# Kernel tuning notes

Hardware: AMD Instinct MI355X
Metric: run time of the kernel (lower is better)

The kernel has to match this reference:

```python
import jax, jax.numpy as jnp
import numpy as np

N = 20000   # nodes per type per hop
E = 200000  # edges per relation per hop
H = 512     # node_feature_hid_len
FU = 512    # raw user feature len
FI = 256    # raw item feature len
NUM_RES = 2
NUM_DNN = 2


def setup_inputs() -> dict:
    key = jax.random.key(0)
    ks = iter(jax.random.split(key, 64))
    p = lambda shape: jax.random.normal(next(ks), shape, dtype=jnp.float32) * 0.05
    inp = {}
    # features per hop per type
    for h in range(3):
        inp[f'feat_user_h{h}'] = jax.random.normal(next(ks), (N, FU), dtype=jnp.float32)
        inp[f'feat_item_h{h}'] = jax.random.normal(next(ks), (N, FI), dtype=jnp.float32)
    del inp['feat_user_h2_']; 


def _unused():
    pass

# rebuild setup_inputs cleanly (above stub replaced)

def setup_inputs() -> dict:
    key = jax.random.key(0)
    ks = iter(jax.random.split(key, 64))
    p = lambda shape: jax.random.normal(next(ks), shape, dtype=jnp.float32) * 0.05
    inp = {}
    for h in range(3):
        inp[f'feat_user_h{h}'] = jax.random.normal(next(ks), (N, FU), dtype=jnp.float32)
        inp[f'feat_item_h{h}'] = jax.random.normal(next(ks), (N, FI), dtype=jnp.float32)
    for name in ('edges_UI_h0', 'edges_IU_h0', 'edges_UI_h1', 'edges_IU_h1'):
        inp[name] = jax.random.randint(next(ks), (2, E), 0, N, dtype=jnp.int32)
    # per-node-type input transforms
    inp['W_user'] = p((FU, H)); inp['b_user'] = jnp.zeros((H,), jnp.float32)
    inp['W_item'] = p((FI, H)); inp['b_item'] = jnp.zeros((H,), jnp.float32)
    # per-relation GATConv params, stacked over 2 relations [UI, IU]
    inp['gat_feat_W'] = p((2, H, H)); inp['gat_feat_b'] = jnp.zeros((2, H), jnp.float32)
    inp['gat_att_w'] = p((2, 2 * H)); inp['gat_att_b'] = jnp.zeros((2,), jnp.float32)
    inp['gat_bias'] = jnp.zeros((2, H), jnp.float32)
    # Res_DNN params
    inp['prep_W'] = p((H, H)); inp['prep_b'] = jnp.zeros((H,), jnp.float32)
    inp['dnn_W'] = p((NUM_RES, NUM_DNN, H, H)); inp['dnn_b'] = jnp.zeros((NUM_RES, NUM_DNN, H), jnp.float32)
    inp['dnn_ln_g'] = jnp.ones((NUM_RES, NUM_DNN, H), jnp.float32); inp['dnn_ln_b'] = jnp.zeros((NUM_RES, NUM_DNN, H), jnp.float32)
    inp['res_ln_g'] = jnp.ones((NUM_RES, H), jnp.float32); inp['res_ln_b'] = jnp.zeros((NUM_RES, H), jnp.float32)
    inp['cls_W'] = p((H, 1)); inp['cls_b'] = jnp.zeros((1,), jnp.float32)
    return inp


def _ln(x, g, b, eps=1e-5):
    mu = jnp.mean(x, axis=-1, keepdims=True)
    var = jnp.mean((x - mu) ** 2, axis=-1, keepdims=True)
    return (x - mu) * jax.lax.rsqrt(var + eps) * g + b


def _gat(head_h, tail_h, edges, fW, fb, aw, ab, bias):
    # GATConv: feat_linear on both sides, tanh edge attention, per-source-row
    # sparse softmax, scatter-weighted sum of transformed tail features.
    s = head_h @ fW + fb            # [Nh, H]
    t = tail_h @ fW + fb            # [Nt, H]
    src, tgt = edges[0], edges[1]
    # att(cat([s_e, t_e])) split into per-node scores (same math as concat @ aw)
    e = jnp.tanh((s @ aw[:H])[src] + (t @ aw[H:])[tgt] + ab)  # [E]
    nh = head_h.shape[0]
    m = jax.ops.segment_max(e, src, num_segments=nh)
    ex = jnp.exp(e - m[src])
    den = jax.ops.segment_sum(ex, src, num_segments=nh)
    alpha = ex / den[src]
    hp = jax.ops.segment_sum(alpha[:, None] * t[tgt], src, num_segments=nh)
    return hp + bias


def _forward(feat_user_h0, feat_item_h0, feat_user_h1, feat_item_h1,
             feat_user_h2, feat_item_h2,
             W_user, b_user, W_item, b_item,
             gat_feat_W, gat_feat_b, gat_att_w, gat_att_b, gat_bias,
             prep_W, prep_b, dnn_W, dnn_b, dnn_ln_g, dnn_ln_b,
             res_ln_g, res_ln_b, cls_W, cls_b,
             edges_UI_h0, edges_IU_h0, edges_UI_h1, edges_IU_h1):
    def gat(r, head, tail, edges):
        return _gat(head, tail, edges, gat_feat_W[r], gat_feat_b[r],
                    gat_att_w[r], gat_att_b[r], gat_bias[r])
    # hop 2 (deepest): transformed source features
    su = feat_user_h2 @ W_user + b_user
    si = feat_item_h2 @ W_item + b_item
    # hop 1
    hu = feat_user_h1 @ W_user + b_user
    hi = feat_item_h1 @ W_item + b_item
    su_new = (hu + gat(0, hu, si, edges_UI_h1)) * 0.5  # mean of [self, UI agg]
    si_new = (hi + gat(1, hi, su, edges_IU_h1)) * 0.5
    su, si = su_new, si_new
    # hop 0
    hu = feat_user_h0 @ W_user + b_user
    hi = feat_item_h0 @ W_item + b_item
    su_new = (hu + gat(0, hu, si, edges_UI_h0)) * 0.5
    su = su_new  # target node type = 'user' (first key)
    # Res_DNN head
    x = su @ prep_W + prep_b
    for r in range(NUM_RES):
        sc = x
        for d in range(NUM_DNN):
            x = _ln(jnp.tanh(x @ dnn_W[r, d] + dnn_b[r, d]), dnn_ln_g[r, d], dnn_ln_b[r, d])
        x = _ln(jnp.tanh(sc + x), res_ln_g[r], res_ln_b[r])
    return jax.nn.sigmoid(x @ cls_W + cls_b)  # [N, 1]


def reference(feat_user_h0, feat_item_h0, feat_user_h1, feat_item_h1,
              feat_user_h2, feat_item_h2,
              edges_UI_h0, edges_IU_h0, edges_UI_h1, edges_IU_h1,
              W_user, b_user, W_item, b_item,
              gat_feat_W, gat_feat_b, gat_att_w, gat_att_b, gat_bias,
              prep_W, prep_b, dnn_W, dnn_b, dnn_ln_g, dnn_ln_b,
              res_ln_g, res_ln_b, cls_W, cls_b):
    return _forward(feat_user_h0, feat_item_h0, feat_user_h1, feat_item_h1,
                    feat_user_h2, feat_item_h2,
                    W_user, b_user, W_item, b_item,
                    gat_feat_W, gat_feat_b, gat_att_w, gat_att_b, gat_bias,
                    prep_W, prep_b, dnn_W, dnn_b, dnn_ln_g, dnn_ln_b,
                    res_ln_g, res_ln_b, cls_W, cls_b,
                    edges_UI_h0, edges_IU_h0, edges_UI_h1, edges_IU_h1)
```

## Files before the change

kernel.cpp:

```cpp
#include <hip/hip_runtime.h>
#include <math.h>

#define NN 20000
#define NE 200000
#define HH 512

typedef __attribute__((ext_vector_type(8))) short short8v;
typedef __attribute__((ext_vector_type(4))) float f32x4;

__device__ inline short f2bf(float f) {
    union { float f; unsigned u; } v; v.f = f;
    unsigned r = (v.u + 0x7fffu + ((v.u >> 16) & 1u)) >> 16;
    return (short)r;
}
__device__ inline float bf2f(short s) {
    union { unsigned u; float f; } v;
    v.u = ((unsigned)(unsigned short)s) << 16;
    return v.f;
}

__device__ inline void gload_lds16(const void* g, void* l) {
    __builtin_amdgcn_global_load_lds(
        (const __attribute__((address_space(1))) void*)g,
        (__attribute__((address_space(3))) void*)l, 16, 0, 0);
}

__global__ __launch_bounds__(256)
void f2b_kernel(const float* __restrict__ src, short* __restrict__ dst, int n8)
{
    int i = blockIdx.x * 256 + threadIdx.x;
    if (i >= n8) return;
    const float4* p = (const float4*)src + (size_t)i * 2;
    float4 a = p[0], b = p[1];
    short8v s;
    s[0] = f2bf(a.x); s[1] = f2bf(a.y); s[2] = f2bf(a.z); s[3] = f2bf(a.w);
    s[4] = f2bf(b.x); s[5] = f2bf(b.y); s[6] = f2bf(b.z); s[7] = f2bf(b.w);
    ((short8v*)dst)[i] = s;
}

__global__ __launch_bounds__(256)
void wtr_kernel(const float* __restrict__ src, short* __restrict__ dst,
                int K, int Ncols)
{
    __shared__ float t[32][33];
    int bx = blockIdx.x * 32;
    int by = blockIdx.y * 32;
    int tx = threadIdx.x, ty = threadIdx.y;
    for (int i = ty; i < 32; i += 8)
        t[i][tx] = src[(size_t)(by + i) * Ncols + bx + tx];
    __syncthreads();
    for (int i = ty; i < 32; i += 8)
        dst[(size_t)(bx + i) * K + by + tx] = f2bf(t[tx][i]);
}

__global__ __launch_bounds__(256)
void mfma_lin(const short* __restrict__ X, const short* __restrict__ WT,
              const float* __restrict__ bias, float* __restrict__ outF,
              short* __restrict__ outB, int M, int K)
{
    __shared__ short8v pool[4096];

    const int tid = threadIdx.x;
    const int lane = tid & 63;
    const int w = tid >> 6;

    const int nby = (M + 127) >> 7;
    const int nwg = nby << 2;
    const int q = nwg >> 3, r = nwg & 7;
    int id = blockIdx.x;
    int xcd = id & 7, wi = id >> 3;
    int wgid = (xcd < r ? xcd * (q + 1) : r * (q + 1) + (xcd - r) * q) + wi;
    const int col0 = (wgid & 3) * 128;
    const int row0 = (wgid >> 2) * 128;

    const int wr = (w >> 1) * 64;
    const int wc = (w & 1) * 64;

    const short* gsrc[8];
#pragma unroll
    for (int g = 0; g < 8; ++g) {
        int p = w * 512 + g * 64 + lane;
        if (p < 1024) {
            int row = p >> 3;
            int c = (p & 7) ^ (row & 7);
            int ga = row0 + row; if (ga >= M) ga = M - 1;
            gsrc[g] = X + (size_t)ga * K + c * 8;
        } else {
            int qq = p - 1024;
            int col = qq >> 3;
            int c = (qq & 7) ^ (col & 7);
            gsrc[g] = WT + (size_t)(col0 + col) * K + c * 8;
        }
    }

    int ar[2][4], br[2][4];
#pragma unroll
    for (int kk = 0; kk < 2; ++kk) {
#pragma unroll
        for (int i = 0; i < 4; ++i) {
            int rr = wr + i * 16 + (lane & 15);
            ar[kk][i] = rr * 8 + ((kk * 4 + (lane >> 4)) ^ (rr & 7));
            int nn = wc + i * 16 + (lane & 15);
            br[kk][i] = 1024 + nn * 8 + ((kk * 4 + (lane >> 4)) ^ (nn & 7));
        }
    }

    f32x4 acc[4][4];
#pragma unroll
    for (int i = 0; i < 4; ++i)
#pragma unroll
        for (int j = 0; j < 4; ++j)
            acc[i][j] = (f32x4){0.f, 0.f, 0.f, 0.f};

    auto stage = [&](int buf, int kk) {
        short8v* base = pool + buf * 2048 + w * 512;
#pragma unroll
        for (int g = 0; g < 8; ++g)
            gload_lds16(gsrc[g] + kk, base + g * 64);
    };

    const int nt = K >> 6;
    stage(0, 0);
    if (nt > 1) stage(1, 64);
    int cur = 0;
    for (int t = 0; t < nt; ++t) {
        if (t + 1 < nt) asm volatile("s_waitcnt vmcnt(8)" ::: "memory");
        else            asm volatile("s_waitcnt vmcnt(0)" ::: "memory");
        __builtin_amdgcn_s_barrier();
        const short8v* S = pool + cur * 2048;
#pragma unroll
        for (int kk = 0; kk < 2; ++kk) {
            short8v af[4], bf[4];
#pragma unroll
            for (int i = 0; i < 4; ++i) af[i] = S[ar[kk][i]];
#pragma unroll
            for (int j = 0; j < 4; ++j) bf[j] = S[br[kk][j]];
#pragma unroll
            for (int i = 0; i < 4; ++i)
#pragma unroll
                for (int j = 0; j < 4; ++j)
                    acc[i][j] = __builtin_amdgcn_mfma_f32_16x16x32_bf16(af[i], bf[j], acc[i][j], 0, 0, 0);
        }
        __builtin_amdgcn_s_barrier();
        if (t + 2 < nt) stage(cur, (t + 2) * 64);
        cur ^= 1;
    }

    float bj[4];
#pragma unroll
    for (int j = 0; j < 4; ++j)
        bj[j] = bias[col0 + wc + j * 16 + (lane & 15)];

    if (outF) {
#pragma unroll
        for (int i = 0; i < 4; ++i) {
#pragma unroll
            for (int rr = 0; rr < 4; ++rr) {
                int row = row0 + wr + i * 16 + (lane >> 4) * 4 + rr;
                if (row < M) {
                    float* op = outF + (size_t)row * HH + col0 + wc + (lane & 15);
#pragma unroll
                    for (int j = 0; j < 4; ++j) op[j * 16] = acc[i][j][rr] + bj[j];
                }
            }
        }
    }
    if (outB) {
        short* lds = (short*)pool + w * 4608;
#pragma unroll
        for (int i = 0; i < 4; ++i)
#pragma unroll
            for (int rr = 0; rr < 4; ++rr) {
                int lrow = i * 16 + (lane >> 4) * 4 + rr;
#pragma unroll
                for (int j = 0; j < 4; ++j)
                    lds[lrow * 72 + j * 16 + (lane & 15)] = f2bf(acc[i][j][rr] + bj[j]);
            }
#pragma unroll
        for (int k = 0; k < 8; ++k) {
            int lr = (lane >> 3) + 8 * k;
            int lc = (lane & 7) * 8;
            int grow = row0 + wr + lr;
            if (grow < M) {
                short8v vv = *(short8v*)(lds + lr * 72 + lc);
                *(short8v*)(outB + (size_t)grow * HH + col0 + wc + lc) = vv;
            }
        }
    }
}

__global__ __launch_bounds__(256)
void gat_pre_kernel(const float* __restrict__ fW, const float* __restrict__ fb,
                    const float* __restrict__ aw, float* __restrict__ uv,
                    float* __restrict__ s0t0)
{
    int row = blockIdx.x * 4 + (threadIdx.x >> 6);
    int lane = threadIdx.x & 63;
    const float4* ah = (const float4*)aw;
    const float4* at = (const float4*)(aw + HH);
    const float4* fp;
    if (row < 512)      fp = (const float4*)(fW + (size_t)row * HH);
    else if (row == 512) fp = (const float4*)fb;
    else return;
    float du = 0.f, dv = 0.f;
#pragma unroll
    for (int l = 0; l < 2; ++l) {
        int idx = lane * 2 + l;
        float4 f = fp[idx], a = ah[idx], b = at[idx];
        du += f.x*a.x + f.y*a.y + f.z*a.z + f.w*a.w;
        dv += f.x*b.x + f.y*b.y + f.z*b.z + f.w*b.w;
    }
#pragma unroll
    for (int m = 32; m >= 1; m >>= 1) {
        du += __shfl_xor(du, m);
        dv += __shfl_xor(dv, m);
    }
    if (lane == 0) {
        if (row < 512) { uv[row] = du; uv[512 + row] = dv; }
        else           { s0t0[0] = du; s0t0[1] = dv; }
    }
}

__global__ __launch_bounds__(256)
void rowdot2_kernel(const short* __restrict__ Hd, const short* __restrict__ Tl,
                    const float* __restrict__ uv, const float* __restrict__ s0t0,
                    float* __restrict__ ss, float* __restrict__ ts, int N)
{
    int row = blockIdx.x * 4 + (threadIdx.x >> 6);
    int lane = threadIdx.x & 63;
    if (row >= N) return;
    short8v h = ((const short8v*)(Hd + (size_t)row * HH))[lane];
    short8v t = ((const short8v*)(Tl + (size_t)row * HH))[lane];
    const float4* up = (const float4*)uv + lane * 2;
    const float4* vp = (const float4*)(uv + HH) + lane * 2;
    float4 u0 = up[0], u1 = up[1], v0 = vp[0], v1 = vp[1];
    float a = bf2f(h[0])*u0.x + bf2f(h[1])*u0.y + bf2f(h[2])*u0.z + bf2f(h[3])*u0.w
            + bf2f(h[4])*u1.x + bf2f(h[5])*u1.y + bf2f(h[6])*u1.z + bf2f(h[7])*u1.w;
    float b = bf2f(t[0])*v0.x + bf2f(t[1])*v0.y + bf2f(t[2])*v0.z + bf2f(t[3])*v0.w
            + bf2f(t[4])*v1.x + bf2f(t[5])*v1.y + bf2f(t[6])*v1.z + bf2f(t[7])*v1.w;
#pragma unroll
    for (int m = 32; m >= 1; m >>= 1) {
        a += __shfl_xor(a, m);
        b += __shfl_xor(b, m);
    }
    if (lane == 0) { ss[row] = a + s0t0[0]; ts[row] = b + s0t0[1]; }
}

__global__ __launch_bounds__(256)
void count2_kernel(const int* __restrict__ s0, const int* __restrict__ s1,
                   int* __restrict__ c0, int* __restrict__ c1, int E)
{
    int i = blockIdx.x * blockDim.x + threadIdx.x;
    if (i < E) atomicAdd(&c0[s0[i]], 1);
    else if (i < 2 * E) atomicAdd(&c1[s1[i - E]], 1);
}

__global__ __launch_bounds__(1024)
void scan2_kernel(const int* __restrict__ c0, const int* __restrict__ c1,
                  int* __restrict__ o0, int* __restrict__ o1,
                  int* __restrict__ u0, int* __restrict__ u1, int n)
{
    const int* counts = blockIdx.x ? c1 : c0;
    int* offs = blockIdx.x ? o1 : o0;
    int* curs = blockIdx.x ? u1 : u0;
    __shared__ int part[1024];
    const int tid = threadIdx.x;
    const int CH = (n + 1023) / 1024;
    const int base = tid * CH;
    int s = 0;
    for (int i = 0; i < CH; ++i) {
        int idx = base + i;
        if (idx < n) s += counts[idx];
    }
    part[tid] = s;
    __syncthreads();
    for (int d = 1; d < 1024; d <<= 1) {
        int v = 0;
        if (tid >= d) v = part[tid - d];
        __syncthreads();
        if (tid >= d) part[tid] += v;
        __syncthreads();
    }
    int run = (tid == 0) ? 0 : part[tid - 1];
    for (int i = 0; i < CH; ++i) {
        int idx = base + i;
        if (idx < n) { offs[idx] = run; curs[idx] = run; run += counts[idx]; }
    }
    if (tid == 1023) offs[n] = run;
}

__global__ __launch_bounds__(256)
void fill_kernel(const int* __restrict__ src, const int* __restrict__ tgt,
                 const float* __restrict__ ss, const float* __restrict__ ts,
                 const float* __restrict__ ab_ptr, int* __restrict__ cursor,
                 int* __restrict__ tvals, float* __restrict__ wv, int E)
{
    int i = blockIdx.x * blockDim.x + threadIdx.x;
    if (i >= E) return;
    int s = src[i], t = tgt[i];
    int pos = atomicAdd(&cursor[s], 1);
    tvals[pos] = t;
    wv[pos] = expf(tanhf(ss[s] + ts[t] + ab_ptr[0]));
}

__global__ __launch_bounds__(256)
void gat_agg_kernel(const int* __restrict__ offs, const int* __restrict__ tvals,
                    const float* __restrict__ wv, const short* __restrict__ T,
                    const short* __restrict__ head, const float* __restrict__ gbias,
                    short* __restrict__ out, int N)
{
    int s = blockIdx.x * 4 + (threadIdx.x >> 6);
    int lane = threadIdx.x & 63;
    if (s >= N) return;
    const int beg = offs[s], end = offs[s + 1];
    float a[8];
#pragma unroll
    for (int q = 0; q < 8; ++q) a[q] = 0.f;
    float den = 0.f;

    int j = beg;
    for (; j + 4 <= end; j += 4) {
        int t0 = tvals[j], t1 = tvals[j + 1], t2 = tvals[j + 2], t3 = tvals[j + 3];
        float w0 = wv[j], w1 = wv[j + 1], w2 = wv[j + 2], w3 = wv[j + 3];
        short8v v0 = ((const short8v*)(T + (size_t)t0 * HH))[lane];
        short8v v1 = ((const short8v*)(T + (size_t)t1 * HH))[lane];
        short8v v2 = ((const short8v*)(T + (size_t)t2 * HH))[lane];
        short8v v3 = ((const short8v*)(T + (size_t)t3 * HH))[lane];
        den += w0 + w1 + w2 + w3;
#pragma unroll
        for (int q = 0; q < 8; ++q) {
            float acc = a[q];
            acc = fmaf(w0, bf2f(v0[q]), acc);
            acc = fmaf(w1, bf2f(v1[q]), acc);
            acc = fmaf(w2, bf2f(v2[q]), acc);
            acc = fmaf(w3, bf2f(v3[q]), acc);
            a[q] = acc;
        }
    }
    for (; j < end; ++j) {
        int t = tvals[j];
        float w = wv[j];
        short8v tv = ((const short8v*)(T + (size_t)t * HH))[lane];
        den += w;
#pragma unroll
        for (int q = 0; q < 8; ++q) a[q] = fmaf(w, bf2f(tv[q]), a[q]);
    }
    float inv = (den > 0.f) ? 1.f / den : 0.f;

    short8v h = ((const short8v*)(head + (size_t)s * HH))[lane];
    const float4* bp = (const float4*)gbias + lane * 2;
    float4 b0 = bp[0], b1 = bp[1];
    float bb[8] = {b0.x, b0.y, b0.z, b0.w, b1.x, b1.y, b1.z, b1.w};
    short8v o;
#pragma unroll
    for (int q = 0; q < 8; ++q)
        o[q] = f2bf((bf2f(h[q]) + a[q] * inv + bb[q]) * 0.5f);
    ((short8v*)(out + (size_t)s * HH))[lane] = o;
}

__global__ __launch_bounds__(256)
void tanh_ln_kernel(const short* __restrict__ Z, const float* __restrict__ res,
                    const float* __restrict__ g, const float* __restrict__ bta,
                    short* __restrict__ outB, float* __restrict__ outF,
                    const float* __restrict__ cWp, const float* __restrict__ cbp,
                    float* __restrict__ outCls, int N)
{
    int row = blockIdx.x * 4 + (threadIdx.x >> 6);
    int lane = threadIdx.x & 63;
    if (row >= N) return;
    short8v zv = ((const short8v*)(Z + (size_t)row * HH))[lane];
    float v[8];
    float sum = 0.f, sum2 = 0.f;
    float rr[8];
    if (res) {
        const float4* rp = (const float4*)(res + (size_t)row * HH) + lane * 2;
        float4 r0 = rp[0], r1 = rp[1];
        rr[0]=r0.x; rr[1]=r0.y; rr[2]=r0.z; rr[3]=r0.w;
        rr[4]=r1.x; rr[5]=r1.y; rr[6]=r1.z; rr[7]=r1.w;
    } else {
#pragma unroll
        for (int q = 0; q < 8; ++q) rr[q] = 0.f;
    }
#pragma unroll
    for (int q = 0; q < 8; ++q) {
        float t = tanhf(bf2f(zv[q]) + rr[q]);
        v[q] = t;
        sum += t;
        sum2 = fmaf(t, t, sum2);
    }
#pragma unroll
    for (int m = 32; m >= 1; m >>= 1) {
        sum  += __shfl_xor(sum, m);
        sum2 += __shfl_xor(sum2, m);
    }
    float mu  = sum * (1.f/HH);
    float var = sum2 * (1.f/HH) - mu*mu;
    float rs  = rsqrtf(var + 1e-5f);
    const float4* gp = (const float4*)g + lane * 2;
    const float4* bp = (const float4*)bta + lane * 2;
    float4 g0 = gp[0], g1 = gp[1], c0 = bp[0], c1 = bp[1];
    float gg[8] = {g0.x, g0.y, g0.z, g0.w, g1.x, g1.y, g1.z, g1.w};
    float cc[8] = {c0.x, c0.y, c0.z, c0.w, c1.x, c1.y, c1.z, c1.w};
    float o[8];
#pragma unroll
    for (int q = 0; q < 8; ++q) o[q] = (v[q]-mu)*rs*gg[q] + cc[q];
    if (outB) {
        short8v ob;
#pragma unroll
        for (int q = 0; q < 8; ++q) ob[q] = f2bf(o[q]);
        ((short8v*)(outB + (size_t)row * HH))[lane] = ob;
    }
    if (outF) {
        float4* op = (float4*)(outF + (size_t)row * HH) + lane * 2;
        op[0] = make_float4(o[0], o[1], o[2], o[3]);
        op[1] = make_float4(o[4], o[5], o[6], o[7]);
    }
    if (cWp) {
        const float4* wp = (const float4*)cWp + lane * 2;
        float4 w0 = wp[0], w1 = wp[1];
        float acc = o[0]*w0.x + o[1]*w0.y + o[2]*w0.z + o[3]*w0.w
                  + o[4]*w1.x + o[5]*w1.y + o[6]*w1.z + o[7]*w1.w;
#pragma unroll
        for (int m = 32; m >= 1; m >>= 1) acc += __shfl_xor(acc, m);
        if (lane == 0) outCls[row] = 1.f / (1.f + expf(-(acc + cbp[0])));
    }
}

extern "C" void kernel_launch(void* const* d_in, const int* in_sizes, int n_in,
                              void* d_out, int out_size, void* d_ws, size_t ws_size,
                              hipStream_t stream)
{
    (void)in_sizes; (void)n_in; (void)out_size; (void)ws_size;
    const int N = NN, E = NE, H = HH;
    const size_t NHf = (size_t)N * H;

    const float* fu0 = (const float*)d_in[0];
    const float* fi1 = (const float*)d_in[3];
    const float* fu2 = (const float*)d_in[4];
    const int* eUI0 = (const int*)d_in[6];
    const int* eIU1 = (const int*)d_in[9];
    const float* Wu  = (const float*)d_in[10];
    const float* bu  = (const float*)d_in[11];
    const float* Wi  = (const float*)d_in[12];
    const float* bi  = (const float*)d_in[13];
    const float* gfW = (const float*)d_in[14];
    const float* gfb = (const float*)d_in[15];
    const float* gaw = (const float*)d_in[16];
    const float* gab = (const float*)d_in[17];
    const float* gbias = (const float*)d_in[18];
    const float* prW = (const float*)d_in[19];
    const float* prb = (const float*)d_in[20];
    const float* dW  = (const float*)d_in[21];
    const float* db  = (const float*)d_in[22];
    const float* dlg = (const float*)d_in[23];
    const float* dlb = (const float*)d_in[24];
    const float* rlg = (const float*)d_in[25];
    const float* rlb = (const float*)d_in[26];
    const float* cW  = (const float*)d_in[27];
    const float* cb  = (const float*)d_in[28];

    float* B5   = (float*)d_ws;
    float* ssb  = B5 + NHf;
    float* tsb  = ssb + N;
    float* uv   = tsb + N;
    float* s0t0 = uv + 1024;
    float* wvb  = s0t0 + 4;
    int* counts0 = (int*)(wvb + E);
    int* counts1 = counts0 + N;
    int* offs0   = counts1 + N;
    int* offs1   = offs0 + N + 1;
    int* cur0    = offs1 + N + 1;
    int* cur1    = cur0 + N;
    int* tvals   = cur1 + N;
    size_t boff = (size_t)((char*)(tvals + E) - (char*)d_ws);
    boff = (boff + 15) & ~(size_t)15;
    short* S0    = (short*)((char*)d_ws + boff);
    short* SUHU  = S0 + 2 * NHf;
    short* XI1   = SUHU + 2 * NHf;
    short* HI    = XI1 + NHf / 2;
    short* SINEW = HI + NHf;
    short* T4    = SINEW + NHf;
    short* SUF   = T4 + NHf;
    short* WTu   = SUF + NHf;
    short* WTi   = WTu + 512 * 512;
    short* WTg0  = WTi + 512 * 256;
    short* WTg1  = WTg0 + 512 * 512;
    short* WTpr  = WTg1 + 512 * 512;
    short* WTd   = WTpr + 512 * 512;
    short* SU  = SUHU;
    short* HU0 = SUHU + NHf;
    short* XB  = SINEW;
    short* ZB  = SU;

    auto WTR = [&](const float* src, short* dst, int K) {
        hipLaunchKernelGGL(wtr_kernel, dim3(16, K / 32), dim3(32, 8), 0, stream,
                           src, dst, K, 512);
    };
    WTR(Wu, WTu, 512);
    WTR(Wi, WTi, 256);
    WTR(gfW, WTg0, 512);
    WTR(gfW + (size_t)H * H, WTg1, 512);
    WTR(prW, WTpr, 512);
    for (int k = 0; k < 4; ++k)
        WTR(dW + (size_t)k * H * H, WTd + (size_t)k * 512 * 512, 512);

    auto F2B = [&](const float* src, short* dst, size_t n) {
        int n8 = (int)(n / 8);
        hipLaunchKernelGGL(f2b_kernel, dim3((n8 + 255) / 256), dim3(256), 0, stream,
                           src, dst, n8);
    };

    hipMemsetAsync(counts0, 0, 2 * N * sizeof(int), stream);
    hipLaunchKernelGGL(count2_kernel, dim3((2 * E + 255) / 256), dim3(256), 0, stream,
                       eUI0, eIU1, counts0, counts1, E);
    hipLaunchKernelGGL(scan2_kernel, dim3(2), dim3(1024), 0, stream,
                       counts0, counts1, offs0, offs1, cur0, cur1, N);

    auto MLIN = [&](const short* X, const short* WT, const float* b,
                    float* oF, short* oB, int M, int K) {
        int nwg = ((M + 127) / 128) * 4;
        hipLaunchKernelGGL(mfma_lin, dim3(nwg), dim3(256), 0, stream,
                           X, WT, b, oF, oB, M, K);
    };
    const int rgrid = (N + 3) / 4;
    const int egrid = (E + 255) / 256;

    auto GAT = [&](int r, const short* headB, const short* tailB, const short* WTg,
                   const int* edges, int* offs, int* curs, short* outB) {
        hipLaunchKernelGGL(gat_pre_kernel, dim3(130), dim3(256), 0, stream,
                           gfW + (size_t)r * H * H, gfb + r * H, gaw + (size_t)r * 2 * H,
                           uv, s0t0);
        MLIN(tailB, WTg, gfb + r * H, nullptr, T4, N, 512);
        hipLaunchKernelGGL(rowdot2_kernel, dim3(rgrid), dim3(256), 0, stream,
                           headB, tailB, uv, s0t0, ssb, tsb, N);
        hipLaunchKernelGGL(fill_kernel, dim3(egrid), dim3(256), 0, stream,
                           edges, edges + E, ssb, tsb, gab + r, curs, tvals, wvb, E);
        hipLaunchKernelGGL(gat_agg_kernel, dim3(rgrid), dim3(256), 0, stream,
                           offs, tvals, wvb, T4, headB, gbias + (size_t)r * H, outB, N);
    };

    F2B(fu2, S0, NHf);
    F2B(fu0, S0 + NHf, NHf);
    F2B(fi1, XI1, NHf / 2);
    MLIN(S0, WTu, bu, nullptr, SUHU, 2 * N, 512);
    MLIN(XI1, WTi, bi, nullptr, HI, N, 256);
    GAT(1, HI, SU, WTg1, eIU1, offs1, cur1, SINEW);
    GAT(0, HU0, SINEW, WTg0, eUI0, offs0, cur0, SUF);

    MLIN(SUF, WTpr, prb, B5, XB, N, 512);
    for (int r = 0; r < 2; ++r) {
        for (int d = 0; d < 2; ++d) {
            MLIN(XB, WTd + (size_t)(r * 2 + d) * 512 * 512, db + (r * 2 + d) * H,
                 nullptr, ZB, N, 512);
            hipLaunchKernelGGL(tanh_ln_kernel, dim3(rgrid), dim3(256), 0, stream,
                               ZB, (const float*)nullptr, dlg + (r * 2 + d) * H,
                               dlb + (r * 2 + d) * H, XB, (float*)nullptr,
                               (const float*)nullptr, (const float*)nullptr,
                               (float*)nullptr, N);
        }
        if (r == 0) {
            hipLaunchKernelGGL(tanh_ln_kernel, dim3(rgrid), dim3(256), 0, stream,
                               XB, B5, rlg, rlb, XB, B5,
                               (const float*)nullptr, (const float*)nullptr,
                               (float*)nullptr, N);
        } else {
            hipLaunchKernelGGL(tanh_ln_kernel, dim3(rgrid), dim3(256), 0, stream,
                               XB, B5, rlg + H, rlb + H, (short*)nullptr,
                               (float*)nullptr, cW, cb, (float*)d_out, N);
        }
    }
}
```

Measured before the change: 561.3 us.

## Batch prep kernels, fuse rowdot into GEMM grid, fuse LN pairs, sort edge buckets

Merges the nine weight-transpose launches and three fp32-to-bf16 conversions into single launches, and runs both GAT attention-vector precomputes in one launch. The row-dot attention scores are computed by extra blocks appended to the GAT GEMM grid, so one launch is saved per relation. The second DNN tanh+LN is fused with the residual tanh+LN. The bf16 GEMM epilogue now stages a full 128x128 tile in LDS with a barrier so stores cover whole tiles. A new per-node sort of CSR buckets by edge index adds work to make the aggregation order deterministic, at the cost of an extra launch and memory traffic.

```diff
diff --git a/kernel.cpp b/kernel.cpp
--- a/kernel.cpp
+++ b/kernel.cpp
@@ -26,28 +26,48 @@
 }
 
 __global__ __launch_bounds__(256)
-void f2b_kernel(const float* __restrict__ src, short* __restrict__ dst, int n8)
+void f2b_all(const float* __restrict__ fu2, const float* __restrict__ fu0,
+             const float* __restrict__ fi1, short* __restrict__ S0,
+             short* __restrict__ XI1, int nh8)
 {
     int i = blockIdx.x * 256 + threadIdx.x;
-    if (i >= n8) return;
-    const float4* p = (const float4*)src + (size_t)i * 2;
+    const float* src; short* dst; int off;
+    if (i < nh8)            { src = fu2; dst = S0;                    off = i; }
+    else if (i < 2 * nh8)   { src = fu0; dst = S0 + (size_t)nh8 * 8;  off = i - nh8; }
+    else if (i < 2 * nh8 + nh8 / 2) { src = fi1; dst = XI1;           off = i - 2 * nh8; }
+    else return;
+    const float4* p = (const float4*)src + (size_t)off * 2;
     float4 a = p[0], b = p[1];
     short8v s;
     s[0] = f2bf(a.x); s[1] = f2bf(a.y); s[2] = f2bf(a.z); s[3] = f2bf(a.w);
     s[4] = f2bf(b.x); s[5] = f2bf(b.y); s[6] = f2bf(b.z); s[7] = f2bf(b.w);
-    ((short8v*)dst)[i] = s;
-}
-
-__global__ __launch_bounds__(256)
-void wtr_kernel(const float* __restrict__ src, short* __restrict__ dst,
-                int K, int Ncols)
+    ((short8v*)dst)[off] = s;
+}
+
+__global__ __launch_bounds__(256)
+void wtr_all(const float* __restrict__ Wu, const float* __restrict__ Wi,
+             const float* __restrict__ gfW, const float* __restrict__ prW,
+             const float* __restrict__ dW,
+             short* __restrict__ WTu, short* __restrict__ WTi,
+             short* __restrict__ WTg0, short* __restrict__ WTg1,
+             short* __restrict__ WTpr, short* __restrict__ WTd)
 {
     __shared__ float t[32][33];
+    int z = blockIdx.z;
+    const float* src; short* dst; int K;
+    if (z == 0)      { src = Wu;  dst = WTu;  K = 512; }
+    else if (z == 1) { src = Wi;  dst = WTi;  K = 256; }
+    else if (z == 2) { src = gfW; dst = WTg0; K = 512; }
+    else if (z == 3) { src = gfW + (size_t)512 * 512; dst = WTg1; K = 512; }
+    else if (z == 4) { src = prW; dst = WTpr; K = 512; }
+    else { src = dW + (size_t)(z - 5) * 512 * 512;
+           dst = WTd + (size_t)(z - 5) * 512 * 512; K = 512; }
+    int by = blockIdx.y * 32;
+    if (by >= K) return;
     int bx = blockIdx.x * 32;
-    int by = blockIdx.y * 32;
     int tx = threadIdx.x, ty = threadIdx.y;
     for (int i = ty; i < 32; i += 8)
-        t[i][tx] = src[(size_t)(by + i) * Ncols + bx + tx];
+        t[i][tx] = src[(size_t)(by + i) * 512 + bx + tx];
     __syncthreads();
     for (int i = ty; i < 32; i += 8)
         dst[(size_t)(bx + i) * K + by + tx] = f2bf(t[tx][i]);
@@ -56,7 +76,10 @@
 __global__ __launch_bounds__(256)
 void mfma_lin(const short* __restrict__ X, const short* __restrict__ WT,
               const float* __restrict__ bias, float* __restrict__ outF,
-              short* __restrict__ outB, int M, int K)
+              short* __restrict__ outB, int M, int K,
+              const short* __restrict__ rdH, const short* __restrict__ rdT,
+              const float* __restrict__ rduv, const float* __restrict__ rds0,
+              float* __restrict__ rdss, float* __restrict__ rdts, int rdN)
 {
     __shared__ short8v pool[4096];
 
@@ -66,8 +89,30 @@
 
     const int nby = (M + 127) >> 7;
     const int nwg = nby << 2;
+    int id = blockIdx.x;
+
+    if (id >= nwg) {
+        int row = (id - nwg) * 4 + w;
+        if (row >= rdN) return;
+        short8v h = ((const short8v*)(rdH + (size_t)row * HH))[lane];
+        short8v t = ((const short8v*)(rdT + (size_t)row * HH))[lane];
+        const float4* up = (const float4*)rduv + lane * 2;
+        const float4* vp = (const float4*)(rduv + HH) + lane * 2;
+        float4 u0 = up[0], u1 = up[1], v0 = vp[0], v1 = vp[1];
+        float a = bf2f(h[0])*u0.x + bf2f(h[1])*u0.y + bf2f(h[2])*u0.z + bf2f(h[3])*u0.w
+                + bf2f(h[4])*u1.x + bf2f(h[5])*u1.y + bf2f(h[6])*u1.z + bf2f(h[7])*u1.w;
+        float b = bf2f(t[0])*v0.x + bf2f(t[1])*v0.y + bf2f(t[2])*v0.z + bf2f(t[3])*v0.w
+                + bf2f(t[4])*v1.x + bf2f(t[5])*v1.y + bf2f(t[6])*v1.z + bf2f(t[7])*v1.w;
+#pragma unroll
+        for (int m = 32; m >= 1; m >>= 1) {
+            a += __shfl_xor(a, m);
+            b += __shfl_xor(b, m);
+        }
+        if (lane == 0) { rdss[row] = a + rds0[0]; rdts[row] = b + rds0[1]; }
+        return;
+    }
+
     const int q = nwg >> 3, r = nwg & 7;
-    int id = blockIdx.x;
     int xcd = id & 7, wi = id >> 3;
     int wgid = (xcd < r ? xcd * (q + 1) : r * (q + 1) + (xcd - r) * q) + wi;
     const int col0 = (wgid & 3) * 128;
@@ -166,40 +211,47 @@
         }
     }
     if (outB) {
-        short* lds = (short*)pool + w * 4608;
+        short* lt = (short*)pool;
 #pragma unroll
         for (int i = 0; i < 4; ++i)
 #pragma unroll
             for (int rr = 0; rr < 4; ++rr) {
-                int lrow = i * 16 + (lane >> 4) * 4 + rr;
+                int lrow = wr + i * 16 + (lane >> 4) * 4 + rr;
 #pragma unroll
                 for (int j = 0; j < 4; ++j)
-                    lds[lrow * 72 + j * 16 + (lane & 15)] = f2bf(acc[i][j][rr] + bj[j]);
+                    lt[lrow * 128 + wc + j * 16 + (lane & 15)] = f2bf(acc[i][j][rr] + bj[j]);
             }
+        __syncthreads();
 #pragma unroll
         for (int k = 0; k < 8; ++k) {
-            int lr = (lane >> 3) + 8 * k;
-            int lc = (lane & 7) * 8;
-            int grow = row0 + wr + lr;
+            int row = (tid >> 4) + 16 * k;
+            int seg = tid & 15;
+            int grow = row0 + row;
             if (grow < M) {
-                short8v vv = *(short8v*)(lds + lr * 72 + lc);
-                *(short8v*)(outB + (size_t)grow * HH + col0 + wc + lc) = vv;
+                short8v vv = *(short8v*)(lt + row * 128 + seg * 8);
+                *(short8v*)(outB + (size_t)grow * HH + col0 + seg * 8) = vv;
             }
         }
     }
 }
 
 __global__ __launch_bounds__(256)
-void gat_pre_kernel(const float* __restrict__ fW, const float* __restrict__ fb,
-                    const float* __restrict__ aw, float* __restrict__ uv,
-                    float* __restrict__ s0t0)
-{
+void gat_pre2(const float* __restrict__ gfW, const float* __restrict__ gfb,
+              const float* __restrict__ gaw, float* __restrict__ uvall,
+              float* __restrict__ s0t0all)
+{
+    int rrel = blockIdx.y;
+    const float* fW = gfW + (size_t)rrel * HH * HH;
+    const float* fb = gfb + rrel * HH;
+    const float* aw = gaw + (size_t)rrel * 2 * HH;
+    float* uv = uvall + rrel * 1024;
+    float* s0t0 = s0t0all + rrel * 4;
     int row = blockIdx.x * 4 + (threadIdx.x >> 6);
     int lane = threadIdx.x & 63;
     const float4* ah = (const float4*)aw;
     const float4* at = (const float4*)(aw + HH);
     const float4* fp;
-    if (row < 512)      fp = (const float4*)(fW + (size_t)row * HH);
+    if (row < 512)       fp = (const float4*)(fW + (size_t)row * HH);
     else if (row == 512) fp = (const float4*)fb;
     else return;
     float du = 0.f, dv = 0.f;
@@ -219,31 +271,6 @@
         if (row < 512) { uv[row] = du; uv[512 + row] = dv; }
         else           { s0t0[0] = du; s0t0[1] = dv; }
     }
-}
-
-__global__ __launch_bounds__(256)
-void rowdot2_kernel(const short* __restrict__ Hd, const short* __restrict__ Tl,
-                    const float* __restrict__ uv, const float* __restrict__ s0t0,
-                    float* __restrict__ ss, float* __restrict__ ts, int N)
-{
-    int row = blockIdx.x * 4 + (threadIdx.x >> 6);
-    int lane = threadIdx.x & 63;
-    if (row >= N) return;
-    short8v h = ((const short8v*)(Hd + (size_t)row * HH))[lane];
-    short8v t = ((const short8v*)(Tl + (size_t)row * HH))[lane];
-    const float4* up = (const float4*)uv + lane * 2;
-    const float4* vp = (const float4*)(uv + HH) + lane * 2;
-    float4 u0 = up[0], u1 = up[1], v0 = vp[0], v1 = vp[1];
-    float a = bf2f(h[0])*u0.x + bf2f(h[1])*u0.y + bf2f(h[2])*u0.z + bf2f(h[3])*u0.w
-            + bf2f(h[4])*u1.x + bf2f(h[5])*u1.y + bf2f(h[6])*u1.z + bf2f(h[7])*u1.w;
-    float b = bf2f(t[0])*v0.x + bf2f(t[1])*v0.y + bf2f(t[2])*v0.z + bf2f(t[3])*v0.w
-            + bf2f(t[4])*v1.x + bf2f(t[5])*v1.y + bf2f(t[6])*v1.z + bf2f(t[7])*v1.w;
-#pragma unroll
-    for (int m = 32; m >= 1; m >>= 1) {
-        a += __shfl_xor(a, m);
-        b += __shfl_xor(b, m);
-    }
-    if (lane == 0) { ss[row] = a + s0t0[0]; ts[row] = b + s0t0[1]; }
 }
 
 __global__ __launch_bounds__(256)
@@ -293,7 +320,8 @@
 void fill_kernel(const int* __restrict__ src, const int* __restrict__ tgt,
                  const float* __restrict__ ss, const float* __restrict__ ts,
                  const float* __restrict__ ab_ptr, int* __restrict__ cursor,
-                 int* __restrict__ tvals, float* __restrict__ wv, int E)
+                 int* __restrict__ tvals, float* __restrict__ wv,
+                 int* __restrict__ eidx, int E)
 {
     int i = blockIdx.x * blockDim.x + threadIdx.x;
     if (i >= E) return;
@@ -301,6 +329,40 @@
     int pos = atomicAdd(&cursor[s], 1);
     tvals[pos] = t;
     wv[pos] = expf(tanhf(ss[s] + ts[t] + ab_ptr[0]));
+    eidx[pos] = i;
+}
+
+__global__ __launch_bounds__(256)
+void sortbkt_kernel(const int* __restrict__ offs, int* __restrict__ tvals,
+                    float* __restrict__ wv, const int* __restrict__ eidx, int N)
+{
+    __shared__ int   lt[4][512];
+    __shared__ float lw[4][512];
+    int w = threadIdx.x >> 6, lane = threadIdx.x & 63;
+    int s = blockIdx.x * 4 + w;
+    if (s >= N) return;
+    int beg = offs[s], end = offs[s + 1];
+    int L = end - beg;
+    if (L <= 1) return;
+    if (L <= 64) {
+        int e = 0x7fffffff, t = 0; float fw = 0.f;
+        if (lane < L) { e = eidx[beg + lane]; t = tvals[beg + lane]; fw = wv[beg + lane]; }
+        int r = 0;
+        for (int k = 0; k < L; ++k) {
+            int ek = __shfl(e, k);
+            r += (ek < e) ? 1 : 0;
+        }
+        if (lane < L) { tvals[beg + r] = t; wv[beg + r] = fw; }
+    } else if (L <= 512) {
+        for (int j = lane; j < L; j += 64) { lt[w][j] = tvals[beg + j]; lw[w][j] = wv[beg + j]; }
+        asm volatile("s_waitcnt lgkmcnt(0) vmcnt(0)" ::: "memory");
+        for (int j = lane; j < L; j += 64) {
+            int e = eidx[beg + j];
+            int r = 0;
+            for (int k = 0; k < L; ++k) r += (eidx[beg + k] < e) ? 1 : 0;
+            tvals[beg + r] = lt[w][j]; wv[beg + r] = lw[w][j];
+        }
+    }
 }
 
 __global__ __launch_bounds__(256)
@@ -359,11 +421,9 @@
 }
 
 __global__ __launch_bounds__(256)
-void tanh_ln_kernel(const short* __restrict__ Z, const float* __restrict__ res,
+void tanh_ln_kernel(const short* __restrict__ Z,
                     const float* __restrict__ g, const float* __restrict__ bta,
-                    short* __restrict__ outB, float* __restrict__ outF,
-                    const float* __restrict__ cWp, const float* __restrict__ cbp,
-                    float* __restrict__ outCls, int N)
+                    short* __restrict__ outB, int N)
 {
     int row = blockIdx.x * 4 + (threadIdx.x >> 6);
     int lane = threadIdx.x & 63;
@@ -371,35 +431,80 @@
     short8v zv = ((const short8v*)(Z + (size_t)row * HH))[lane];
     float v[8];
     float sum = 0.f, sum2 = 0.f;
-    float rr[8];
-    if (res) {
-        const float4* rp = (const float4*)(res + (size_t)row * HH) + lane * 2;
-        float4 r0 = rp[0], r1 = rp[1];
-        rr[0]=r0.x; rr[1]=r0.y; rr[2]=r0.z; rr[3]=r0.w;
-        rr[4]=r1.x; rr[5]=r1.y; rr[6]=r1.z; rr[7]=r1.w;
-    } else {
-#pragma unroll
-        for (int q = 0; q < 8; ++q) rr[q] = 0.f;
-    }
 #pragma unroll
     for (int q = 0; q < 8; ++q) {
-        float t = tanhf(bf2f(zv[q]) + rr[q]);
-        v[q] = t;
-        sum += t;
-        sum2 = fmaf(t, t, sum2);
+        float t = tanhf(bf2f(zv[q]));
+        v[q] = t; sum += t; sum2 = fmaf(t, t, sum2);
     }
 #pragma unroll
     for (int m = 32; m >= 1; m >>= 1) {
-        sum  += __shfl_xor(sum, m);
-        sum2 += __shfl_xor(sum2, m);
-    }
-    float mu  = sum * (1.f/HH);
-    float var = sum2 * (1.f/HH) - mu*mu;
-    float rs  = rsqrtf(var + 1e-5f);
+        sum += __shfl_xor(sum, m); sum2 += __shfl_xor(sum2, m);
+    }
+    float mu = sum * (1.f/HH);
+    float rs = rsqrtf(sum2 * (1.f/HH) - mu*mu + 1e-5f);
     const float4* gp = (const float4*)g + lane * 2;
     const float4* bp = (const float4*)bta + lane * 2;
     float4 g0 = gp[0], g1 = gp[1], c0 = bp[0], c1 = bp[1];
     float gg[8] = {g0.x, g0.y, g0.z, g0.w, g1.x, g1.y, g1.z, g1.w};
+    float cc[8] = {c0.x, c0.y, c0.z, c0.w, c1.x, c1.y, c1.z, c1.w};
+    short8v ob;
+#pragma unroll
+    for (int q = 0; q < 8; ++q) ob[q] = f2bf((v[q]-mu)*rs*gg[q] + cc[q]);
+    ((short8v*)(outB + (size_t)row * HH))[lane] = ob;
+}
+
+__global__ __launch_bounds__(256)
+void tanh_ln2_kernel(const short* __restrict__ Z, const float* __restrict__ sc,
+                     const float* __restrict__ g1, const float* __restrict__ b1,
+                     const float* __restrict__ g2, const float* __restrict__ b2,
+                     short* __restrict__ outB, float* __restrict__ outF,
+                     const float* __restrict__ cWp, const float* __restrict__ cbp,
+                     float* __restrict__ outCls, int N)
+{
+    int row = blockIdx.x * 4 + (threadIdx.x >> 6);
+    int lane = threadIdx.x & 63;
+    if (row >= N) return;
+    short8v zv = ((const short8v*)(Z + (size_t)row * HH))[lane];
+    float v[8];
+    float sum = 0.f, sum2 = 0.f;
+#pragma unroll
+    for (int q = 0; q < 8; ++q) {
+        float t = tanhf(bf2f(zv[q]));
+        v[q] = t; sum += t; sum2 = fmaf(t, t, sum2);
+    }
+#pragma unroll
+    for (int m = 32; m >= 1; m >>= 1) {
+        sum += __shfl_xor(sum, m); sum2 += __shfl_xor(sum2, m);
+    }
+    float mu = sum * (1.f/HH);
+    float rs = rsqrtf(sum2 * (1.f/HH) - mu*mu + 1e-5f);
+    {
+        const float4* gp = (const float4*)g1 + lane * 2;
+        const float4* bp = (const float4*)b1 + lane * 2;
+        float4 g0 = gp[0], g1v = gp[1], c0 = bp[0], c1 = bp[1];
+        float gg[8] = {g0.x, g0.y, g0.z, g0.w, g1v.x, g1v.y, g1v.z, g1v.w};
+        float cc[8] = {c0.x, c0.y, c0.z, c0.w, c1.x, c1.y, c1.z, c1.w};
+        const float4* sp = (const float4*)(sc + (size_t)row * HH) + lane * 2;
+        float4 s0 = sp[0], s1 = sp[1];
+        float ssv[8] = {s0.x, s0.y, s0.z, s0.w, s1.x, s1.y, s1.z, s1.w};
+        sum = 0.f; sum2 = 0.f;
+#pragma unroll
+        for (int q = 0; q < 8; ++q) {
+            float x2 = (v[q]-mu)*rs*gg[q] + cc[q];
+            float t = tanhf(ssv[q] + x2);
+            v[q] = t; sum += t; sum2 = fmaf(t, t, sum2);
+        }
+    }
+#pragma unroll
+    for (int m = 32; m >= 1; m >>= 1) {
+        sum += __shfl_xor(sum, m); sum2 += __shfl_xor(sum2, m);
+    }
+    mu = sum * (1.f/HH);
+    rs = rsqrtf(sum2 * (1.f/HH) - mu*mu + 1e-5f);
+    const float4* gp = (const float4*)g2 + lane * 2;
+    const float4* bp = (const float4*)b2 + lane * 2;
+    float4 g0 = gp[0], g1v = gp[1], c0 = bp[0], c1 = bp[1];
+    float gg[8] = {g0.x, g0.y, g0.z, g0.w, g1v.x, g1v.y, g1v.z, g1v.w};
     float cc[8] = {c0.x, c0.y, c0.z, c0.w, c1.x, c1.y, c1.z, c1.w};
     float o[8];
 #pragma unroll
@@ -459,12 +564,12 @@
     const float* cW  = (const float*)d_in[27];
     const float* cb  = (const float*)d_in[28];
 
-    float* B5   = (float*)d_ws;
-    float* ssb  = B5 + NHf;
-    float* tsb  = ssb + N;
-    float* uv   = tsb + N;
-    float* s0t0 = uv + 1024;
-    float* wvb  = s0t0 + 4;
+    float* B5     = (float*)d_ws;
+    float* ssb    = B5 + NHf;
+    float* tsb    = ssb + N;
+    float* uvall  = tsb + N;
+    float* s0t0a  = uvall + 2048;
+    float* wvb    = s0t0a + 8;
     int* counts0 = (int*)(wvb + E);
     int* counts1 = counts0 + N;
     int* offs0   = counts1 + N;
@@ -472,7 +577,8 @@
     int* cur0    = offs1 + N + 1;
     int* cur1    = cur0 + N;
     int* tvals   = cur1 + N;
-    size_t boff = (size_t)((char*)(tvals + E) - (char*)d_ws);
+    int* eidxb   = tvals + E;
+    size_t boff = (size_t)((char*)(eidxb + E) - (char*)d_ws);
     boff = (boff + 15) & ~(size_t)15;
     short* S0    = (short*)((char*)d_ws + boff);
     short* SUHU  = S0 + 2 * NHf;
@@ -492,81 +598,69 @@
     short* XB  = SINEW;
     short* ZB  = SU;
 
-    auto WTR = [&](const float* src, short* dst, int K) {
-        hipLaunchKernelGGL(wtr_kernel, dim3(16, K / 32), dim3(32, 8), 0, stream,
-                           src, dst, K, 512);
-    };
-    WTR(Wu, WTu, 512);
-    WTR(Wi, WTi, 256);
-    WTR(gfW, WTg0, 512);
-    WTR(gfW + (size_t)H * H, WTg1, 512);
-    WTR(prW, WTpr, 512);
-    for (int k = 0; k < 4; ++k)
-        WTR(dW + (size_t)k * H * H, WTd + (size_t)k * 512 * 512, 512);
-
-    auto F2B = [&](const float* src, short* dst, size_t n) {
-        int n8 = (int)(n / 8);
-        hipLaunchKernelGGL(f2b_kernel, dim3((n8 + 255) / 256), dim3(256), 0, stream,
-                           src, dst, n8);
-    };
-
+    hipLaunchKernelGGL(wtr_all, dim3(16, 16, 9), dim3(32, 8), 0, stream,
+                       Wu, Wi, gfW, prW, dW, WTu, WTi, WTg0, WTg1, WTpr, WTd);
+    int nh8 = (int)(NHf / 8);
+    int ftot = 2 * nh8 + nh8 / 2;
+    hipLaunchKernelGGL(f2b_all, dim3((ftot + 255) / 256), dim3(256), 0, stream,
+                       fu2, fu0, fi1, S0, XI1, nh8);
     hipMemsetAsync(counts0, 0, 2 * N * sizeof(int), stream);
     hipLaunchKernelGGL(count2_kernel, dim3((2 * E + 255) / 256), dim3(256), 0, stream,
                        eUI0, eIU1, counts0, counts1, E);
     hipLaunchKernelGGL(scan2_kernel, dim3(2), dim3(1024), 0, stream,
                        counts0, counts1, offs0, offs1, cur0, cur1, N);
-
-    auto MLIN = [&](const short* X, const short* WT, const float* b,
-                    float* oF, short* oB, int M, int K) {
-        int nwg = ((M + 127) / 128) * 4;
-        hipLaunchKernelGGL(mfma_lin, dim3(nwg), dim3(256), 0, stream,
-                           X, WT, b, oF, oB, M, K);
-    };
+    hipLaunchKernelGGL(gat_pre2, dim3(130, 2), dim3(256), 0, stream,
+                       gfW, gfb, gaw, uvall, s0t0a);
+
     const int rgrid = (N + 3) / 4;
     const int egrid = (E + 255) / 256;
+    auto MLIN = [&](const short* X, const short* WT, const float* b,
+                    float* oF, short* oB, int M, int K,
+                    const short* rdH, const short* rdT, const float* rduv,
+                    const float* rds0) {
+        int nwg = ((M + 127) / 128) * 4;
+        int grid = nwg + (rdH ? rgrid : 0);
+        hipLaunchKernelGGL(mfma_lin, dim3(grid), dim3(256), 0, stream,
+                           X, WT, b, oF, oB, M, K,
+                           rdH, rdT, rduv, rds0, ssb, tsb, N);
+    };
 
     auto GAT = [&](int r, const short* headB, const short* tailB, const short* WTg,
                    const int* edges, int* offs, int* curs, short* outB) {
-        hipLaunchKernelGGL(gat_pre_kernel, dim3(130), dim3(256), 0, stream,
-                           gfW + (size_t)r * H * H, gfb + r * H, gaw + (size_t)r * 2 * H,
-                           uv, s0t0);
-        MLIN(tailB, WTg, gfb + r * H, nullptr, T4, N, 512);
-        hipLaunchKernelGGL(rowdot2_kernel, dim3(rgrid), dim3(256), 0, stream,
-                           headB, tailB, uv, s0t0, ssb, tsb, N);
+        MLIN(tailB, WTg, gfb + r * H, nullptr, T4, N, 512,
+             headB, tailB, uvall + r * 1024, s0t0a + r * 4);
         hipLaunchKernelGGL(fill_kernel, dim3(egrid), dim3(256), 0, stream,
-                           edges, edges + E, ssb, tsb, gab + r, curs, tvals, wvb, E);
+                           edges, edges + E, ssb, tsb, gab + r, curs, tvals, wvb,
+                           eidxb, E);
+        hipLaunchKernelGGL(sortbkt_kernel, dim3(rgrid), dim3(256), 0, stream,
+                           offs, tvals, wvb, eidxb, N);
         hipLaunchKernelGGL(gat_agg_kernel, dim3(rgrid), dim3(256), 0, stream,
                            offs, tvals, wvb, T4, headB, gbias + (size_t)r * H, outB, N);
     };
 
-    F2B(fu2, S0, NHf);
-    F2B(fu0, S0 + NHf, NHf);
-    F2B(fi1, XI1, NHf / 2);
-    MLIN(S0, WTu, bu, nullptr, SUHU, 2 * N, 512);
-    MLIN(XI1, WTi, bi, nullptr, HI, N, 256);
+    MLIN(S0, WTu, bu, nullptr, SUHU, 2 * N, 512, nullptr, nullptr, nullptr, nullptr);
+    MLIN(XI1, WTi, bi, nullptr, HI, N, 256, nullptr, nullptr, nullptr, nullptr);
     GAT(1, HI, SU, WTg1, eIU1, offs1, cur1, SINEW);
     GAT(0, HU0, SINEW, WTg0, eUI0, offs0, cur0, SUF);
 
-    MLIN(SUF, WTpr, prb, B5, XB, N, 512);
+    MLIN(SUF, WTpr, prb, B5, XB, N, 512, nullptr, nullptr, nullptr, nullptr);
     for (int r = 0; r < 2; ++r) {
-        for (int d = 0; d < 2; ++d) {
-            MLIN(XB, WTd + (size_t)(r * 2 + d) * 512 * 512, db + (r * 2 + d) * H,
-                 nullptr, ZB, N, 512);
-            hipLaunchKernelGGL(tanh_ln_kernel, dim3(rgrid), dim3(256), 0, stream,
-                               ZB, (const float*)nullptr, dlg + (r * 2 + d) * H,
-                               dlb + (r * 2 + d) * H, XB, (float*)nullptr,
-                               (const float*)nullptr, (const float*)nullptr,
-                               (float*)nullptr, N);
-        }
+        MLIN(XB, WTd + (size_t)(r * 2) * 512 * 512, db + (r * 2) * H,
+             nullptr, ZB, N, 512, nullptr, nullptr, nullptr, nullptr);
+        hipLaunchKernelGGL(tanh_ln_kernel, dim3(rgrid), dim3(256), 0, stream,
+                           ZB, dlg + (r * 2) * H, dlb + (r * 2) * H, XB, N);
+        MLIN(XB, WTd + (size_t)(r * 2 + 1) * 512 * 512, db + (r * 2 + 1) * H,
+             nullptr, ZB, N, 512, nullptr, nullptr, nullptr, nullptr);
         if (r == 0) {
-            hipLaunchKernelGGL(tanh_ln_kernel, dim3(rgrid), dim3(256), 0, stream,
-                               XB, B5, rlg, rlb, XB, B5,
-                               (const float*)nullptr, (const float*)nullptr,
+            hipLaunchKernelGGL(tanh_ln2_kernel, dim3(rgrid), dim3(256), 0, stream,
+                               ZB, B5, dlg + H, dlb + H, rlg, rlb,
+                               XB, B5, (const float*)nullptr, (const float*)nullptr,
                                (float*)nullptr, N);
         } else {
-            hipLaunchKernelGGL(tanh_ln_kernel, dim3(rgrid), dim3(256), 0, stream,
-                               XB, B5, rlg + H, rlb + H, (short*)nullptr,
-                               (float*)nullptr, cW, cb, (float*)d_out, N);
-        }
-    }
-}
+            hipLaunchKernelGGL(tanh_ln2_kernel, dim3(rgrid), dim3(256), 0, stream,
+                               ZB, B5, dlg + 3 * H, dlb + 3 * H, rlg + H, rlb + H,
+                               (short*)nullptr, (float*)nullptr, cW, cb,
+                               (float*)d_out, N);
+        }
+    }
+}
```

After: 516.1 us. -8.1%, faster.
